# Kernel tuning notes

Measured on AMD Instinct MI355X. Metric: run time of the kernel, lower is better.

Reference implementation:

```python
import jax, jax.numpy as jnp
import numpy as np

B, N, D_IN, D_HID, D_OUT = 4096, 64, 128, 128, 128


def setup_inputs() -> dict:
    key = jax.random.key(0)
    k1, k2, k3, k4, k5, k6 = jax.random.split(key, 6)
    inp = jax.random.normal(k1, (B, D_IN), dtype=jnp.float32)
    neigh = jax.random.normal(k2, (B, N, D_IN), dtype=jnp.float32)
    # zero out some neighbors so the mask path is exercised
    drop = jax.random.bernoulli(k3, 0.2, (B, N))
    neigh = jnp.where(drop[:, :, None], 0.0, neigh)
    W_mlp = jax.random.normal(k4, (D_HID, D_IN), dtype=jnp.float32) * (1.0 / np.sqrt(D_IN))
    b_mlp = jnp.zeros((D_HID,), dtype=jnp.float32)
    W_comb = jax.random.normal(k5, (2 * D_OUT, D_IN + D_HID), dtype=jnp.float32) * (1.0 / np.sqrt(D_IN + D_HID))
    b_comb = jax.random.normal(k6, (2 * D_OUT,), dtype=jnp.float32) * 0.01
    return {"input": inp, "neighbor_inputs": neigh, "W_mlp": W_mlp, "b_mlp": b_mlp,
            "W_comb": W_comb, "b_comb": b_comb}


def reference(input, neighbor_inputs, W_mlp, b_mlp, W_comb, b_comb):
    # mask: neighbors whose features sum to exactly 0 (padding)  [B, N, 1]
    mask = (jnp.sum(neighbor_inputs, axis=-1) == 0.0)[:, :, None]
    # per-neighbor MLP + ReLU: [B, N, D_HID]
    h = jax.nn.relu(jnp.einsum('bnd,hd->bnh', neighbor_inputs, W_mlp) + b_mlp)
    h = jnp.where(mask, 0.0, h)
    # max-pool over neighbor dim -> [B, D_HID]
    pooled = jnp.max(h, axis=1)
    # combine: concat + linear + ReLU -> [B, 2*D_OUT]
    combined = jnp.concatenate([input, pooled], axis=-1)
    out = jax.nn.relu(combined @ W_comb.T + b_comb)
    return out
```

## Files before the change

kernel.cpp:

```cpp
#include <hip/hip_runtime.h>
#include <hip/hip_bf16.h>

typedef __attribute__((ext_vector_type(4))) float f32x4;
typedef __attribute__((ext_vector_type(8))) short bf16x8;

#define N_NEI 64
#define D_IN  128
#define D_HID 128

__device__ __forceinline__ unsigned bfbits(float f) {
  unsigned u = __float_as_uint(f);
  return (u + 0x7fffu + ((u >> 16) & 1u)) >> 16;
}

union BF8 { bf16x8 v; unsigned u[4]; };

__device__ __forceinline__ bf16x8 pack8(const float4& a, const float4& b) {
  BF8 r;
  r.u[0] = bfbits(a.x) | (bfbits(a.y) << 16);
  r.u[1] = bfbits(a.z) | (bfbits(a.w) << 16);
  r.u[2] = bfbits(b.x) | (bfbits(b.y) << 16);
  r.u[3] = bfbits(b.z) | (bfbits(b.w) << 16);
  return r.v;
}

__global__ __launch_bounds__(256, 4)
void k1_pool(const float* __restrict__ neigh, const float* __restrict__ Wmlp,
             const float* __restrict__ bmlp, unsigned short* __restrict__ pooled) {
  __shared__ unsigned short Wl[D_HID * D_IN];
  __shared__ float pool[4][D_HID];

  const int tid = threadIdx.x;
  const int l = tid & 63;
  const int w = tid >> 6;

  const float4* W4 = (const float4*)Wmlp;
  #pragma unroll
  for (int it = 0; it < 8; ++it) {
    int f8 = it * 256 + tid;
    int j  = f8 >> 4;
    int d0 = (f8 & 15) * 8;
    float4 a = W4[f8 * 2];
    float4 b = W4[f8 * 2 + 1];
    int byte = j * 256 + ((d0 * 2) ^ ((j & 7) << 4));
    *(bf16x8*)((char*)Wl + byte) = pack8(a, b);
  }

  const int lr = l & 15;
  const int lg = l >> 4;

  float bml[8];
  #pragma unroll
  for (int t = 0; t < 8; ++t) bml[t] = bmlp[t * 16 + lr];

  __syncthreads();

  for (int i = 0; i < 4; ++i) {
    const int b = blockIdx.x * 4 + i;
    const float* arow = neigh + (size_t)(b * N_NEI + w * 16 + lr) * D_IN + lg * 8;

    bf16x8 af[4];
    float rs = 0.f;
    #pragma unroll
    for (int ks = 0; ks < 4; ++ks) {
      float4 a0 = *(const float4*)(arow + ks * 32);
      float4 a1 = *(const float4*)(arow + ks * 32 + 4);
      rs += a0.x + a0.y + a0.z + a0.w + a1.x + a1.y + a1.z + a1.w;
      af[ks] = pack8(a0, a1);
    }
    rs += __shfl_xor(rs, 16);
    rs += __shfl_xor(rs, 32);
    unsigned mask16 = (unsigned)(__ballot(rs == 0.0f) & 0xFFFFull);

    f32x4 acc[8];
    #pragma unroll
    for (int t = 0; t < 8; ++t) acc[t] = (f32x4){0.f, 0.f, 0.f, 0.f};

    #pragma unroll
    for (int t = 0; t < 8; ++t) {
      #pragma unroll
      for (int ks = 0; ks < 4; ++ks) {
        int jr = t * 16 + lr;
        int d0 = ks * 32 + lg * 8;
        bf16x8 bf = *(const bf16x8*)((const char*)Wl + jr * 256 + ((d0 * 2) ^ ((jr & 7) << 4)));
        acc[t] = __builtin_amdgcn_mfma_f32_16x16x32_bf16(af[ks], bf, acc[t], 0, 0, 0);
      }
    }

    #pragma unroll
    for (int t = 0; t < 8; ++t) {
      float mt = 0.f;
      #pragma unroll
      for (int r = 0; r < 4; ++r) {
        int row = lg * 4 + r;
        float v = fmaxf(acc[t][r] + bml[t], 0.f);
        if ((mask16 >> row) & 1u) v = 0.f;
        mt = fmaxf(mt, v);
      }
      mt = fmaxf(mt, __shfl_xor(mt, 16));
      mt = fmaxf(mt, __shfl_xor(mt, 32));
      if (l < 16) pool[w][t * 16 + l] = mt;
    }
    __syncthreads();
    if (tid < 128) {
      float p0 = fmaxf(pool[0][tid], pool[1][tid]);
      float p1 = fmaxf(pool[2][tid], pool[3][tid]);
      pooled[(size_t)b * D_HID + tid] = (unsigned short)bfbits(fmaxf(p0, p1));
    }
    __syncthreads();
  }
}

__global__ __launch_bounds__(256, 4)
void k2_comb(const float* __restrict__ inp, const unsigned short* __restrict__ pooled,
             const float* __restrict__ Wcomb, const float* __restrict__ bcomb,
             float* __restrict__ out) {
  __shared__ unsigned short Wl[64 * 256];

  const int tid = threadIdx.x;
  const int l = tid & 63;
  const int w = tid >> 6;
  const int mchunk = blockIdx.x >> 2;
  const int colq   = blockIdx.x & 3;

  const float4* W4 = (const float4*)Wcomb;
  #pragma unroll
  for (int it = 0; it < 8; ++it) {
    int c  = it * 256 + tid;
    int jr = c >> 5;
    int d0 = (c & 31) * 8;
    int gidx = ((colq * 64 + jr) * 256 + d0) >> 2;
    float4 a = W4[gidx];
    float4 b = W4[gidx + 1];
    int byte = jr * 512 + ((d0 * 2) ^ ((jr & 7) << 4));
    *(bf16x8*)((char*)Wl + byte) = pack8(a, b);
  }

  const int lr = l & 15;
  const int lg = l >> 4;

  float bcl[4];
  #pragma unroll
  for (int t = 0; t < 4; ++t) bcl[t] = bcomb[colq * 64 + t * 16 + lr];

  __syncthreads();

  const int row = mchunk * 64 + w * 16 + lr;

  bf16x8 af[8];
  #pragma unroll
  for (int ks = 0; ks < 4; ++ks) {
    const float* p = inp + (size_t)row * 128 + ks * 32 + lg * 8;
    float4 a0 = *(const float4*)p;
    float4 a1 = *(const float4*)(p + 4);
    af[ks] = pack8(a0, a1);
  }
  #pragma unroll
  for (int ks = 4; ks < 8; ++ks) {
    af[ks] = *(const bf16x8*)(pooled + (size_t)row * 128 + (ks - 4) * 32 + lg * 8);
  }

  f32x4 acc[4];
  #pragma unroll
  for (int t = 0; t < 4; ++t) acc[t] = (f32x4){0.f, 0.f, 0.f, 0.f};
  #pragma unroll
  for (int t = 0; t < 4; ++t) {
    #pragma unroll
    for (int ks = 0; ks < 8; ++ks) {
      int jr = t * 16 + lr;
      int d0 = ks * 32 + lg * 8;
      bf16x8 bf = *(const bf16x8*)((const char*)Wl + jr * 512 + ((d0 * 2) ^ ((jr & 7) << 4)));
      acc[t] = __builtin_amdgcn_mfma_f32_16x16x32_bf16(af[ks], bf, acc[t], 0, 0, 0);
    }
  }

  #pragma unroll
  for (int t = 0; t < 4; ++t) {
    #pragma unroll
    for (int r = 0; r < 4; ++r) {
      int ro = mchunk * 64 + w * 16 + lg * 4 + r;
      int co = colq * 64 + t * 16 + lr;
      float v = acc[t][r] + bcl[t];
      out[(size_t)ro * 256 + co] = fmaxf(v, 0.f);
    }
  }
}

extern "C" void kernel_launch(void* const* d_in, const int* in_sizes, int n_in,
                              void* d_out, int out_size, void* d_ws, size_t ws_size,
                              hipStream_t stream) {
  const float* inp   = (const float*)d_in[0];
  const float* neigh = (const float*)d_in[1];
  const float* Wmlp  = (const float*)d_in[2];
  const float* bmlp  = (const float*)d_in[3];
  const float* Wcomb = (const float*)d_in[4];
  const float* bcomb = (const float*)d_in[5];
  float* out = (float*)d_out;
  unsigned short* pooled = (unsigned short*)d_ws;

  k1_pool<<<1024, 256, 0, stream>>>(neigh, Wmlp, bmlp, pooled);
  k2_comb<<<256, 256, 0, stream>>>(inp, pooled, Wcomb, bcomb, out);
}
```

Measured before the change: 39.53 us.

## Assign one batch row per wave in pool kernel, removing per-row block syncs

The pooling kernel now gives each wave a whole batch element: the wave loops over four 16-neighbor tiles and keeps a running max in registers. The cross-wave shared-memory reduction and the two __syncthreads per batch row go away, leaving a single sync and a vectorized bf16x2 store. The manual bf16 rounding is also replaced by the HIP __float22bfloat162_rn intrinsic. In exchange each wave carries more unrolled work and more live registers across the tile loop.

```diff
diff --git a/kernel.cpp b/kernel.cpp
--- a/kernel.cpp
+++ b/kernel.cpp
@@ -8,19 +8,14 @@
 #define D_IN  128
 #define D_HID 128
 
-__device__ __forceinline__ unsigned bfbits(float f) {
-  unsigned u = __float_as_uint(f);
-  return (u + 0x7fffu + ((u >> 16) & 1u)) >> 16;
-}
-
-union BF8 { bf16x8 v; unsigned u[4]; };
+union BF8 { bf16x8 v; __hip_bfloat162 h[4]; unsigned u[4]; };
 
 __device__ __forceinline__ bf16x8 pack8(const float4& a, const float4& b) {
   BF8 r;
-  r.u[0] = bfbits(a.x) | (bfbits(a.y) << 16);
-  r.u[1] = bfbits(a.z) | (bfbits(a.w) << 16);
-  r.u[2] = bfbits(b.x) | (bfbits(b.y) << 16);
-  r.u[3] = bfbits(b.z) | (bfbits(b.w) << 16);
+  r.h[0] = __float22bfloat162_rn(float2{a.x, a.y});
+  r.h[1] = __float22bfloat162_rn(float2{a.z, a.w});
+  r.h[2] = __float22bfloat162_rn(float2{b.x, b.y});
+  r.h[3] = __float22bfloat162_rn(float2{b.z, b.w});
   return r.v;
 }
 
@@ -28,7 +23,7 @@
 void k1_pool(const float* __restrict__ neigh, const float* __restrict__ Wmlp,
              const float* __restrict__ bmlp, unsigned short* __restrict__ pooled) {
   __shared__ unsigned short Wl[D_HID * D_IN];
-  __shared__ float pool[4][D_HID];
+  __shared__ float pscr[4][D_HID];
 
   const int tid = threadIdx.x;
   const int l = tid & 63;
@@ -55,9 +50,16 @@
 
   __syncthreads();
 
-  for (int i = 0; i < 4; ++i) {
-    const int b = blockIdx.x * 4 + i;
-    const float* arow = neigh + (size_t)(b * N_NEI + w * 16 + lr) * D_IN + lg * 8;
+  const int b = blockIdx.x * 4 + w;
+  const float* rowbase = neigh + (size_t)b * N_NEI * D_IN;
+
+  float pmax[8];
+  #pragma unroll
+  for (int t = 0; t < 8; ++t) pmax[t] = 0.f;
+
+  #pragma unroll
+  for (int mt = 0; mt < 4; ++mt) {
+    const float* arow = rowbase + (size_t)(mt * 16 + lr) * D_IN + lg * 8;
 
     bf16x8 af[4];
     float rs = 0.f;
@@ -89,26 +91,30 @@
 
     #pragma unroll
     for (int t = 0; t < 8; ++t) {
-      float mt = 0.f;
       #pragma unroll
       for (int r = 0; r < 4; ++r) {
         int row = lg * 4 + r;
         float v = fmaxf(acc[t][r] + bml[t], 0.f);
         if ((mask16 >> row) & 1u) v = 0.f;
-        mt = fmaxf(mt, v);
+        pmax[t] = fmaxf(pmax[t], v);
       }
-      mt = fmaxf(mt, __shfl_xor(mt, 16));
-      mt = fmaxf(mt, __shfl_xor(mt, 32));
-      if (l < 16) pool[w][t * 16 + l] = mt;
-    }
-    __syncthreads();
-    if (tid < 128) {
-      float p0 = fmaxf(pool[0][tid], pool[1][tid]);
-      float p1 = fmaxf(pool[2][tid], pool[3][tid]);
-      pooled[(size_t)b * D_HID + tid] = (unsigned short)bfbits(fmaxf(p0, p1));
-    }
-    __syncthreads();
-  }
+    }
+  }
+
+  #pragma unroll
+  for (int t = 0; t < 8; ++t) {
+    pmax[t] = fmaxf(pmax[t], __shfl_xor(pmax[t], 16));
+    pmax[t] = fmaxf(pmax[t], __shfl_xor(pmax[t], 32));
+  }
+
+  if (l < 16) {
+    #pragma unroll
+    for (int t = 0; t < 8; ++t) pscr[w][t * 16 + l] = pmax[t];
+  }
+  __syncthreads();
+  float2 pv = *(const float2*)&pscr[w][2 * l];
+  __hip_bfloat162 h2 = __float22bfloat162_rn(pv);
+  ((unsigned*)(pooled + (size_t)b * D_HID))[l] = *(unsigned*)&h2;
 }
 
 __global__ __launch_bounds__(256, 4)
```

Result: slower. 109.3 us (+176.5%).
